# Kernel optimization log

Measured on AMD Instinct MI355X. Metric: run time of the kernel, lower is better.

Reference implementation:

```python
import jax, jax.numpy as jnp
import numpy as np

LOG_2PI = np.float32(np.log(2.0 * np.pi))
NEG_BIG = np.float32(-9e15)


def setup_inputs() -> dict:
    key = jax.random.key(0)
    ks = jax.random.split(key, 8)
    N, F_in, F_out, H = 8192, 512, 128, 16
    x = jax.random.normal(ks[0], (N, F_in), dtype=jnp.float32)
    adj = jax.random.randint(ks[1], (N, N), 0, 2, dtype=jnp.int32)
    # xavier_uniform-ish init for W (gain 1.414)
    lim = np.float32(1.414 * np.sqrt(6.0 / (F_in + F_out)))
    W = jax.random.uniform(ks[2], (F_in, F_out), jnp.float32, -lim, lim)
    # VariationalAttentionNet params: lin1(2*F_out -> H), lin21/lin22(H -> 1)
    w1 = jax.random.normal(ks[3], (H, 2 * F_out), dtype=jnp.float32) * 0.05
    b1 = jnp.zeros((H,), jnp.float32)
    w21 = jax.random.normal(ks[4], (1, H), dtype=jnp.float32) * 0.05
    b21 = jnp.zeros((1,), jnp.float32)
    w22 = jax.random.normal(ks[5], (1, H), dtype=jnp.float32) * 0.05
    b22 = jnp.zeros((1,), jnp.float32)
    return {"x": x, "adj": adj, "W": W, "w1": w1, "b1": b1,
            "w21": w21, "b21": b21, "w22": w22, "b22": b22}


def reference(x, adj, W, w1, b1, w21, b21, w22, b22):
    # h = x @ W  [N, F_out]
    h = x @ W
    # VariationalAttentionNet(h, h), eval mode: z = mu
    u = jax.nn.relu(jnp.concatenate([h, h], axis=1) @ w1.T + b1)  # [N, H]
    mu = u @ w21.T + b21   # [N, 1]
    lv = u @ w22.T + b22   # [N, 1]
    sigma = jax.nn.softplus(lv)
    z = mu
    # qmp = -(log p(z) - log q(z)); with z = mu, log q(mu) = -log(sigma) - 0.5*log(2pi)
    log_p = jnp.sum(-0.5 * z * z - 0.5 * LOG_2PI)
    log_q = jnp.sum(-jnp.log(sigma) - 0.5 * LOG_2PI)
    qmp = log_q - log_p
    # per-node score z broadcast across row, masked by adjacency, row softmax
    scores = jnp.where(adj > 0, z, NEG_BIG)          # [N, N]
    attention = jax.nn.softmax(scores, axis=1)       # [N, N] (dropout off in eval)
    h_prime = attention @ h                          # [N, F_out]
    return jax.nn.elu(h_prime), qmp
```

## Files before the change

### kernel.cpp

```cpp
#include <hip/hip_runtime.h>

typedef unsigned int u32;
typedef unsigned short u16;

#define NN 8192
#define FIN 512
#define FOUT 128
#define NH 16
#define BK 64
#define BKA 256

typedef float f32x16 __attribute__((ext_vector_type(16)));
typedef __bf16 bf16x8 __attribute__((ext_vector_type(8)));

union PackAB { u32 u[4]; bf16x8 v; };

__device__ __forceinline__ u32 rne_hi(u32 u) {
  return u + (0x7FFFu + ((u >> 16) & 1u));
}
__device__ __forceinline__ u16 f32_to_bf16(float f) {
  return (u16)(rne_hi(__float_as_uint(f)) >> 16);
}

__global__ __launch_bounds__(256) void prep_kernel(
    const float* __restrict__ W, const float* __restrict__ w1,
    u16* __restrict__ WT, float* __restrict__ w1s) {
  int b = blockIdx.x, t = threadIdx.x;
  if (b < 256) {
    int o = b * 256 + t;
    int n = o >> 9, k = o & 511;
    WT[o] = f32_to_bf16(W[k * FOUT + n]);
  } else {
    for (int e = t; e < NH * FOUT; e += 256) {
      int k = e >> 7, f = e & 127;
      w1s[e] = w1[k * 256 + f] + w1[k * 256 + 128 + f];
    }
  }
}

__global__ __launch_bounds__(256, 6) void h_kernel(
    const float* __restrict__ x, const u16* __restrict__ WT,
    float* __restrict__ Hp, int KL) {
  __shared__ u16 aS[32 * BK];
  __shared__ u16 bS[128 * BK];
  int t = threadIdx.x;
  int w = t >> 6, l = t & 63;
  int m = l & 31, kh = l >> 5;
  int tile = blockIdx.x & 255, chunk = blockIdx.x >> 8;
  int i0 = tile * 32, k0 = chunk * KL;

  int arow = t >> 4, acol = (t & 15) * 4;
  int ac = (t & 15) >> 1, ah = t & 1;
  int aoff0 = arow * BK + ((ac ^ (arow & 7)) << 3) + ah * 4;
  int aoff1 = (arow + 16) * BK + ((ac ^ ((arow + 16) & 7)) << 3) + ah * 4;
  const float* ap0 = x + (size_t)(i0 + arow) * FIN + k0 + acol;
  const float* ap1 = ap0 + (size_t)16 * FIN;
  int hr = t >> 3, hc = t & 7;
  const u16* bp0 = WT + (size_t)hr * FIN + k0 + hc * 8;
  int boff[4];
#pragma unroll
  for (int p = 0; p < 4; ++p) {
    int r = hr + 32 * p;
    boff[p] = r * BK + ((hc ^ (r & 7)) << 3);
  }
  int aro = m * BK, am7 = m & 7;
  int nB = w * 32 + m;
  int bro = nB * BK, bm7 = nB & 7;

  f32x16 acc;
#pragma unroll
  for (int r = 0; r < 16; ++r) acc[r] = 0.0f;

  for (int o = 0; o < KL; o += BK) {
    float4 a0 = *(const float4*)ap0;
    float4 a1 = *(const float4*)ap1;
    uint4 h0 = *(const uint4*)bp0;
    uint4 h1 = *(const uint4*)(bp0 + 32 * (size_t)FIN);
    uint4 h2 = *(const uint4*)(bp0 + 64 * (size_t)FIN);
    uint4 h3 = *(const uint4*)(bp0 + 96 * (size_t)FIN);
    ap0 += BK; ap1 += BK; bp0 += BK;
    uint2 w0, w1v;
    w0.x = (rne_hi(__float_as_uint(a0.y)) & 0xFFFF0000u) | (rne_hi(__float_as_uint(a0.x)) >> 16);
    w0.y = (rne_hi(__float_as_uint(a0.w)) & 0xFFFF0000u) | (rne_hi(__float_as_uint(a0.z)) >> 16);
    w1v.x = (rne_hi(__float_as_uint(a1.y)) & 0xFFFF0000u) | (rne_hi(__float_as_uint(a1.x)) >> 16);
    w1v.y = (rne_hi(__float_as_uint(a1.w)) & 0xFFFF0000u) | (rne_hi(__float_as_uint(a1.z)) >> 16);
    *(uint2*)&aS[aoff0] = w0;
    *(uint2*)&aS[aoff1] = w1v;
    *(uint4*)&bS[boff[0]] = h0;
    *(uint4*)&bS[boff[1]] = h1;
    *(uint4*)&bS[boff[2]] = h2;
    *(uint4*)&bS[boff[3]] = h3;
    __syncthreads();
#pragma unroll
    for (int s = 0; s < BK; s += 16) {
      int cA = (s >> 3) + kh;
      PackAB pa, pb;
      pa.v = *(const bf16x8*)&aS[aro + ((cA ^ am7) << 3)];
      pb.v = *(const bf16x8*)&bS[bro + ((cA ^ bm7) << 3)];
      acc = __builtin_amdgcn_mfma_f32_32x32x16_bf16(pa.v, pb.v, acc, 0, 0, 0);
    }
    __syncthreads();
  }
  float* hp = Hp + (size_t)chunk * NN * FOUT;
  int col = w * 32 + m;
#pragma unroll
  for (int r = 0; r < 16; ++r) {
    int row = (r & 3) + 8 * (r >> 2) + 4 * kh;
    hp[(size_t)(i0 + row) * FOUT + col] = acc[r];
  }
}

__global__ __launch_bounds__(256) void reduceH_kernel(
    const float* __restrict__ Hp, int KSH,
    const float* __restrict__ b1, const float* __restrict__ w21,
    const float* __restrict__ b21, const float* __restrict__ w22,
    const float* __restrict__ b22, const float* __restrict__ w1s,
    u16* __restrict__ HTf, float* __restrict__ qpart) {
  __shared__ float hs[32][FOUT + 4];
  __shared__ float w1l[NH][FOUT + 4];
  __shared__ float us[32][NH + 1];
  int t = threadIdx.x;
  int i0 = blockIdx.x * 32;
  float v[16];
  const float* base = Hp + (size_t)i0 * FOUT + t * 16;
#pragma unroll
  for (int e = 0; e < 16; e += 4) {
    float4 x4 = *(const float4*)(base + e);
    v[e] = x4.x; v[e + 1] = x4.y; v[e + 2] = x4.z; v[e + 3] = x4.w;
  }
  for (int c = 1; c < KSH; ++c) {
    const float* p = base + (size_t)c * NN * FOUT;
#pragma unroll
    for (int e = 0; e < 16; e += 4) {
      float4 x4 = *(const float4*)(p + e);
      v[e] += x4.x; v[e + 1] += x4.y; v[e + 2] += x4.z; v[e + 3] += x4.w;
    }
  }
  {
    int row = t >> 3, c0 = (t & 7) * 16;
#pragma unroll
    for (int e = 0; e < 16; ++e) hs[row][c0 + e] = v[e];
  }
  for (int e = t; e < NH * FOUT; e += 256) w1l[e >> 7][e & 127] = w1s[e];
  __syncthreads();
  {
    int n = t & 127, g2 = t >> 7;
#pragma unroll
    for (int gg = 0; gg < 2; ++gg) {
      int g = g2 + 2 * gg;
      int k16 = (i0 >> 4) + (g >> 1), kh = g & 1;
      u32 p[4];
#pragma unroll
      for (int j = 0; j < 4; ++j) {
        u16 lo = f32_to_bf16(hs[g * 8 + 2 * j][n]);
        u16 hi = f32_to_bf16(hs[g * 8 + 2 * j + 1][n]);
        p[j] = (u32)lo | ((u32)hi << 16);
      }
      uint4 st; st.x = p[0]; st.y = p[1]; st.z = p[2]; st.w = p[3];
      size_t off = ((size_t)(k16 * 4 + (n >> 5)) * 64 + kh * 32 + (n & 31)) * 8;
      *(uint4*)(HTf + off) = st;
    }
  }
  {
    int i = t >> 3, p = t & 7;
    float s0 = b1[p], s1 = b1[p + 8];
#pragma unroll 4
    for (int f = 0; f < FOUT; ++f) {
      float hv = hs[i][f];
      s0 = fmaf(hv, w1l[p][f], s0);
      s1 = fmaf(hv, w1l[p + 8][f], s1);
    }
    us[i][p] = fmaxf(s0, 0.0f);
    us[i][p + 8] = fmaxf(s1, 0.0f);
  }
  __syncthreads();
  if (t < 32) {
    float mu = b21[0], lv = b22[0];
#pragma unroll
    for (int k = 0; k < NH; ++k) {
      mu = fmaf(us[t][k], w21[k], mu);
      lv = fmaf(us[t][k], w22[k], lv);
    }
    float sp = fmaxf(lv, 0.0f) + log1pf(expf(-fabsf(lv)));
    float q = 0.5f * mu * mu - logf(sp);
#pragma unroll
    for (int off = 16; off; off >>= 1) q += __shfl_down(q, off);
    if (t == 0) qpart[blockIdx.x] = q;
  }
}

__global__ __launch_bounds__(256, 4) void attn_kernel(
    const int* __restrict__ adj, const u16* __restrict__ HTf,
    float* __restrict__ Sp, u32* __restrict__ degw, int KL) {
  __shared__ u16 aS[32 * BKA];
  int t = threadIdx.x;
  int w = t >> 6, l = t & 63;
  int m = l & 31, kh = l >> 5;
  int tile = blockIdx.x & 255, chunk = blockIdx.x >> 8;
  int i0 = tile * 32, k0 = chunk * KL;

  int ar = t >> 3, lc = t & 7;
  const int* apb = adj + (size_t)(i0 + ar) * NN + k0 + lc * 4;
  int woff[8];
#pragma unroll
  for (int q = 0; q < 8; ++q) {
    int c = q * 4 + (lc >> 1);
    woff[q] = ar * 256 + (((c ^ ar) & 31) << 3) + (lc & 1) * 4;
  }
  const u16* bp = HTf + ((size_t)(k0 >> 4) * 4 * 64 + (size_t)(w * 64 + l)) * 8;

  f32x16 acc;
#pragma unroll
  for (int r = 0; r < 16; ++r) acc[r] = 0.0f;
  u32 degacc = 0;

  int nslab = KL / BKA;
  int4 aC[8], aN[8];
#pragma unroll
  for (int q = 0; q < 8; ++q) aC[q] = *(const int4*)(apb + q * 32);
  apb += BKA;

  for (int o = 0; o < nslab; ++o) {
    if (o) __syncthreads();
#pragma unroll
    for (int q = 0; q < 8; ++q) {
      u32 p0 = ((u32)aC[q].y << 16) | (u32)aC[q].x;
      u32 p1 = ((u32)aC[q].w << 16) | (u32)aC[q].z;
      degacc += p0 + p1;
      uint2 wv; wv.x = p0 * 0x3F80u; wv.y = p1 * 0x3F80u;
      *(uint2*)&aS[woff[q]] = wv;
    }
    __syncthreads();
    if (o + 1 < nslab) {
#pragma unroll
      for (int q = 0; q < 8; ++q) aN[q] = *(const int4*)(apb + q * 32);
      apb += BKA;
    }
    {
      bf16x8 bF[4];
#pragma unroll
      for (int j = 0; j < 4; ++j) bF[j] = *(const bf16x8*)(bp + j * 2048);
#pragma unroll
      for (int k16 = 0; k16 < 16; k16 += 4) {
        bf16x8 bN[4];
        if (k16 + 4 < 16) {
#pragma unroll
          for (int j = 0; j < 4; ++j)
            bN[j] = *(const bf16x8*)(bp + (k16 + 4 + j) * 2048);
        }
#pragma unroll
        for (int j = 0; j < 4; ++j) {
          int cc = (k16 + j) * 2 + kh;
          PackAB pa;
          pa.v = *(const bf16x8*)&aS[m * 256 + (((cc ^ m) & 31) << 3)];
          acc = __builtin_amdgcn_mfma_f32_32x32x16_bf16(pa.v, bF[j], acc, 0, 0, 0);
        }
#pragma unroll
        for (int j = 0; j < 4; ++j) bF[j] = bN[j];
      }
    }
    bp += (size_t)16 * 2048;
#pragma unroll
    for (int q = 0; q < 8; ++q) aC[q] = aN[q];
  }
  u32 d = (degacc & 0xFFFFu) + (degacc >> 16);
  d += __shfl_down(d, 4);
  d += __shfl_down(d, 2);
  d += __shfl_down(d, 1);
  if (lc == 0) degw[chunk * NN + i0 + ar] = d;
  float* sp = Sp + (size_t)chunk * NN * FOUT;
  int col = w * 32 + m;
#pragma unroll
  for (int r = 0; r < 16; ++r) {
    int row = (r & 3) + 8 * (r >> 2) + 4 * kh;
    sp[(size_t)(i0 + row) * FOUT + col] = acc[r];
  }
}

__global__ __launch_bounds__(256) void reduceSq_kernel(
    const float* __restrict__ Sp, const u32* __restrict__ degw,
    const float* __restrict__ qpart, float* __restrict__ out, int KSA) {
  int t = threadIdx.x;
  if (blockIdx.x == 1024) {
    __shared__ float sred[4];
    float v = qpart[t];
#pragma unroll
    for (int off = 32; off; off >>= 1) v += __shfl_down(v, off);
    if ((t & 63) == 0) sred[t >> 6] = v;
    __syncthreads();
    if (t == 0) out[(size_t)NN * FOUT] = sred[0] + sred[1] + sred[2] + sred[3];
    return;
  }
  int idx = (blockIdx.x * 256 + t) * 4;
  int i = idx >> 7;
  u32 deg = 0;
  for (int c = 0; c < KSA; ++c) deg += degw[c * NN + i];
  float4 s = {0.0f, 0.0f, 0.0f, 0.0f};
  for (int c = 0; c < KSA; ++c) {
    float4 v4 = *(const float4*)(Sp + (size_t)c * NN * FOUT + idx);
    s.x += v4.x; s.y += v4.y; s.z += v4.z; s.w += v4.w;
  }
  float rd = deg ? 1.0f / (float)deg : 0.0f;
  float4 o;
  o.x = s.x * rd; o.y = s.y * rd; o.z = s.z * rd; o.w = s.w * rd;
  o.x = o.x > 0.0f ? o.x : expm1f(o.x);
  o.y = o.y > 0.0f ? o.y : expm1f(o.y);
  o.z = o.z > 0.0f ? o.z : expm1f(o.z);
  o.w = o.w > 0.0f ? o.w : expm1f(o.w);
  *(float4*)(out + idx) = o;
}

extern "C" void kernel_launch(void* const* d_in, const int* in_sizes, int n_in,
                              void* d_out, int out_size, void* d_ws, size_t ws_size,
                              hipStream_t stream) {
  (void)in_sizes; (void)n_in; (void)out_size;
  const float* x   = (const float*)d_in[0];
  const int*   adj = (const int*)d_in[1];
  const float* W   = (const float*)d_in[2];
  const float* w1  = (const float*)d_in[3];
  const float* b1  = (const float*)d_in[4];
  const float* w21 = (const float*)d_in[5];
  const float* b21 = (const float*)d_in[6];
  const float* w22 = (const float*)d_in[7];
  const float* b22 = (const float*)d_in[8];
  float* out = (float*)d_out;

  const size_t TILE4 = (size_t)NN * FOUT * 4;
  int KSA = 4, KSH = 4;
  for (;;) {
    size_t need = (size_t)(KSA + KSH) * TILE4
                + (size_t)NN * FOUT * 2
                + (size_t)FOUT * FIN * 2
                + (size_t)KSA * NN * 4
                + NH * FOUT * 4 + 2048;
    if (need <= ws_size || (KSA == 1 && KSH == 1)) break;
    if (KSH > 1) KSH >>= 1; else KSA >>= 1;
  }

  char* ws = (char*)d_ws;
  float* Sp   = (float*)ws;                          ws += (size_t)KSA * TILE4;
  float* Hp   = (float*)ws;                          ws += (size_t)KSH * TILE4;
  u16*   HTf  = (u16*)ws;                            ws += (size_t)NN * FOUT * 2;
  u16*   WT   = (u16*)ws;                            ws += (size_t)FOUT * FIN * 2;
  u32*   degw = (u32*)ws;                            ws += (size_t)KSA * NN * 4;
  float* w1s  = (float*)ws;                          ws += NH * FOUT * 4;
  float* qpart= (float*)ws;

  prep_kernel<<<257, 256, 0, stream>>>(W, w1, WT, w1s);
  h_kernel<<<256 * KSH, 256, 0, stream>>>(x, WT, Hp, FIN / KSH);
  reduceH_kernel<<<256, 256, 0, stream>>>(Hp, KSH, b1, w21, b21, w22, b22, w1s, HTf, qpart);
  attn_kernel<<<256 * KSA, 256, 0, stream>>>(adj, HTf, Sp, degw, NN / KSA);
  reduceSq_kernel<<<1025, 256, 0, stream>>>(Sp, degw, qpart, out, KSA);
}
```

Before: 419.0 us.

## Drop split-K partials and fuse reductions into the GEMM and attention kernels

```diff
diff --git a/kernel.cpp b/kernel.cpp
--- a/kernel.cpp
+++ b/kernel.cpp
@@ -38,25 +38,31 @@
   }
 }
 
-__global__ __launch_bounds__(256, 6) void h_kernel(
+__global__ __launch_bounds__(256) void h_fused_kernel(
     const float* __restrict__ x, const u16* __restrict__ WT,
-    float* __restrict__ Hp, int KL) {
-  __shared__ u16 aS[32 * BK];
-  __shared__ u16 bS[128 * BK];
+    const float* __restrict__ b1, const float* __restrict__ w21,
+    const float* __restrict__ b21, const float* __restrict__ w22,
+    const float* __restrict__ b22, const float* __restrict__ w1s,
+    u16* __restrict__ HTf, float* __restrict__ qpart) {
+  __shared__ union {
+    struct { u16 aS[32 * BK]; u16 bS[128 * BK]; } g;
+    float hs[32][FOUT + 4];
+  } S;
+  __shared__ float w1l[NH][FOUT + 4];
+  __shared__ float us[32][NH + 1];
   int t = threadIdx.x;
   int w = t >> 6, l = t & 63;
   int m = l & 31, kh = l >> 5;
-  int tile = blockIdx.x & 255, chunk = blockIdx.x >> 8;
-  int i0 = tile * 32, k0 = chunk * KL;
+  int i0 = blockIdx.x * 32;
 
   int arow = t >> 4, acol = (t & 15) * 4;
   int ac = (t & 15) >> 1, ah = t & 1;
   int aoff0 = arow * BK + ((ac ^ (arow & 7)) << 3) + ah * 4;
   int aoff1 = (arow + 16) * BK + ((ac ^ ((arow + 16) & 7)) << 3) + ah * 4;
-  const float* ap0 = x + (size_t)(i0 + arow) * FIN + k0 + acol;
+  const float* ap0 = x + (size_t)(i0 + arow) * FIN + acol;
   const float* ap1 = ap0 + (size_t)16 * FIN;
   int hr = t >> 3, hc = t & 7;
-  const u16* bp0 = WT + (size_t)hr * FIN + k0 + hc * 8;
+  const u16* bp0 = WT + (size_t)hr * FIN + hc * 8;
   int boff[4];
 #pragma unroll
   for (int p = 0; p < 4; ++p) {
@@ -67,79 +73,60 @@
   int nB = w * 32 + m;
   int bro = nB * BK, bm7 = nB & 7;
 
+  float4 xa[8], xb[8];
+#pragma unroll
+  for (int o = 0; o < 8; ++o) {
+    xa[o] = *(const float4*)(ap0 + o * BK);
+    xb[o] = *(const float4*)(ap1 + o * BK);
+  }
+  uint4 hC[4], hN[4];
+#pragma unroll
+  for (int j = 0; j < 4; ++j) hC[j] = *(const uint4*)(bp0 + (size_t)(32 * j) * FIN);
+  bp0 += BK;
+
   f32x16 acc;
 #pragma unroll
   for (int r = 0; r < 16; ++r) acc[r] = 0.0f;
 
-  for (int o = 0; o < KL; o += BK) {
-    float4 a0 = *(const float4*)ap0;
-    float4 a1 = *(const float4*)ap1;
-    uint4 h0 = *(const uint4*)bp0;
-    uint4 h1 = *(const uint4*)(bp0 + 32 * (size_t)FIN);
-    uint4 h2 = *(const uint4*)(bp0 + 64 * (size_t)FIN);
-    uint4 h3 = *(const uint4*)(bp0 + 96 * (size_t)FIN);
-    ap0 += BK; ap1 += BK; bp0 += BK;
+#pragma unroll
+  for (int o = 0; o < 8; ++o) {
+    if (o) __syncthreads();
     uint2 w0, w1v;
-    w0.x = (rne_hi(__float_as_uint(a0.y)) & 0xFFFF0000u) | (rne_hi(__float_as_uint(a0.x)) >> 16);
-    w0.y = (rne_hi(__float_as_uint(a0.w)) & 0xFFFF0000u) | (rne_hi(__float_as_uint(a0.z)) >> 16);
-    w1v.x = (rne_hi(__float_as_uint(a1.y)) & 0xFFFF0000u) | (rne_hi(__float_as_uint(a1.x)) >> 16);
-    w1v.y = (rne_hi(__float_as_uint(a1.w)) & 0xFFFF0000u) | (rne_hi(__float_as_uint(a1.z)) >> 16);
-    *(uint2*)&aS[aoff0] = w0;
-    *(uint2*)&aS[aoff1] = w1v;
-    *(uint4*)&bS[boff[0]] = h0;
-    *(uint4*)&bS[boff[1]] = h1;
-    *(uint4*)&bS[boff[2]] = h2;
-    *(uint4*)&bS[boff[3]] = h3;
+    w0.x = (rne_hi(__float_as_uint(xa[o].y)) & 0xFFFF0000u) | (rne_hi(__float_as_uint(xa[o].x)) >> 16);
+    w0.y = (rne_hi(__float_as_uint(xa[o].w)) & 0xFFFF0000u) | (rne_hi(__float_as_uint(xa[o].z)) >> 16);
+    w1v.x = (rne_hi(__float_as_uint(xb[o].y)) & 0xFFFF0000u) | (rne_hi(__float_as_uint(xb[o].x)) >> 16);
+    w1v.y = (rne_hi(__float_as_uint(xb[o].w)) & 0xFFFF0000u) | (rne_hi(__float_as_uint(xb[o].z)) >> 16);
+    *(uint2*)&S.g.aS[aoff0] = w0;
+    *(uint2*)&S.g.aS[aoff1] = w1v;
+#pragma unroll
+    for (int j = 0; j < 4; ++j) *(uint4*)&S.g.bS[boff[j]] = hC[j];
     __syncthreads();
+    if (o + 1 < 8) {
+#pragma unroll
+      for (int j = 0; j < 4; ++j) hN[j] = *(const uint4*)(bp0 + (size_t)(32 * j) * FIN);
+      bp0 += BK;
+    }
 #pragma unroll
     for (int s = 0; s < BK; s += 16) {
       int cA = (s >> 3) + kh;
       PackAB pa, pb;
-      pa.v = *(const bf16x8*)&aS[aro + ((cA ^ am7) << 3)];
-      pb.v = *(const bf16x8*)&bS[bro + ((cA ^ bm7) << 3)];
+      pa.v = *(const bf16x8*)&S.g.aS[aro + ((cA ^ am7) << 3)];
+      pb.v = *(const bf16x8*)&S.g.bS[bro + ((cA ^ bm7) << 3)];
       acc = __builtin_amdgcn_mfma_f32_32x32x16_bf16(pa.v, pb.v, acc, 0, 0, 0);
     }
-    __syncthreads();
-  }
-  float* hp = Hp + (size_t)chunk * NN * FOUT;
-  int col = w * 32 + m;
-#pragma unroll
-  for (int r = 0; r < 16; ++r) {
-    int row = (r & 3) + 8 * (r >> 2) + 4 * kh;
-    hp[(size_t)(i0 + row) * FOUT + col] = acc[r];
-  }
-}
-
-__global__ __launch_bounds__(256) void reduceH_kernel(
-    const float* __restrict__ Hp, int KSH,
-    const float* __restrict__ b1, const float* __restrict__ w21,
-    const float* __restrict__ b21, const float* __restrict__ w22,
-    const float* __restrict__ b22, const float* __restrict__ w1s,
-    u16* __restrict__ HTf, float* __restrict__ qpart) {
-  __shared__ float hs[32][FOUT + 4];
-  __shared__ float w1l[NH][FOUT + 4];
-  __shared__ float us[32][NH + 1];
-  int t = threadIdx.x;
-  int i0 = blockIdx.x * 32;
-  float v[16];
-  const float* base = Hp + (size_t)i0 * FOUT + t * 16;
-#pragma unroll
-  for (int e = 0; e < 16; e += 4) {
-    float4 x4 = *(const float4*)(base + e);
-    v[e] = x4.x; v[e + 1] = x4.y; v[e + 2] = x4.z; v[e + 3] = x4.w;
-  }
-  for (int c = 1; c < KSH; ++c) {
-    const float* p = base + (size_t)c * NN * FOUT;
-#pragma unroll
-    for (int e = 0; e < 16; e += 4) {
-      float4 x4 = *(const float4*)(p + e);
-      v[e] += x4.x; v[e + 1] += x4.y; v[e + 2] += x4.z; v[e + 3] += x4.w;
-    }
-  }
+    if (o + 1 < 8) {
+#pragma unroll
+      for (int j = 0; j < 4; ++j) hC[j] = hN[j];
+    }
+  }
+  __syncthreads();
   {
-    int row = t >> 3, c0 = (t & 7) * 16;
-#pragma unroll
-    for (int e = 0; e < 16; ++e) hs[row][c0 + e] = v[e];
+    int col = w * 32 + m;
+#pragma unroll
+    for (int r = 0; r < 16; ++r) {
+      int row = (r & 3) + 8 * (r >> 2) + 4 * kh;
+      S.hs[row][col] = acc[r];
+    }
   }
   for (int e = t; e < NH * FOUT; e += 256) w1l[e >> 7][e & 127] = w1s[e];
   __syncthreads();
@@ -148,16 +135,16 @@
 #pragma unroll
     for (int gg = 0; gg < 2; ++gg) {
       int g = g2 + 2 * gg;
-      int k16 = (i0 >> 4) + (g >> 1), kh = g & 1;
+      int k16 = (i0 >> 4) + (g >> 1), khh = g & 1;
       u32 p[4];
 #pragma unroll
       for (int j = 0; j < 4; ++j) {
-        u16 lo = f32_to_bf16(hs[g * 8 + 2 * j][n]);
-        u16 hi = f32_to_bf16(hs[g * 8 + 2 * j + 1][n]);
+        u16 lo = f32_to_bf16(S.hs[g * 8 + 2 * j][n]);
+        u16 hi = f32_to_bf16(S.hs[g * 8 + 2 * j + 1][n]);
         p[j] = (u32)lo | ((u32)hi << 16);
       }
       uint4 st; st.x = p[0]; st.y = p[1]; st.z = p[2]; st.w = p[3];
-      size_t off = ((size_t)(k16 * 4 + (n >> 5)) * 64 + kh * 32 + (n & 31)) * 8;
+      size_t off = ((size_t)(k16 * 4 + (n >> 5)) * 64 + khh * 32 + (n & 31)) * 8;
       *(uint4*)(HTf + off) = st;
     }
   }
@@ -166,7 +153,7 @@
     float s0 = b1[p], s1 = b1[p + 8];
 #pragma unroll 4
     for (int f = 0; f < FOUT; ++f) {
-      float hv = hs[i][f];
+      float hv = S.hs[i][f];
       s0 = fmaf(hv, w1l[p][f], s0);
       s1 = fmaf(hv, w1l[p + 8][f], s1);
     }
@@ -189,32 +176,32 @@
   }
 }
 
-__global__ __launch_bounds__(256, 4) void attn_kernel(
+__global__ __launch_bounds__(256) void attn_kernel(
     const int* __restrict__ adj, const u16* __restrict__ HTf,
-    float* __restrict__ Sp, u32* __restrict__ degw, int KL) {
+    const float* __restrict__ qpart, float* __restrict__ out) {
   __shared__ u16 aS[32 * BKA];
+  __shared__ float dinv[32];
   int t = threadIdx.x;
   int w = t >> 6, l = t & 63;
   int m = l & 31, kh = l >> 5;
-  int tile = blockIdx.x & 255, chunk = blockIdx.x >> 8;
-  int i0 = tile * 32, k0 = chunk * KL;
+  int i0 = blockIdx.x * 32;
 
   int ar = t >> 3, lc = t & 7;
-  const int* apb = adj + (size_t)(i0 + ar) * NN + k0 + lc * 4;
+  const int* apb = adj + (size_t)(i0 + ar) * NN + lc * 4;
   int woff[8];
 #pragma unroll
   for (int q = 0; q < 8; ++q) {
     int c = q * 4 + (lc >> 1);
     woff[q] = ar * 256 + (((c ^ ar) & 31) << 3) + (lc & 1) * 4;
   }
-  const u16* bp = HTf + ((size_t)(k0 >> 4) * 4 * 64 + (size_t)(w * 64 + l)) * 8;
+  const u16* bp = HTf + (size_t)(w * 64 + l) * 8;
 
   f32x16 acc;
 #pragma unroll
   for (int r = 0; r < 16; ++r) acc[r] = 0.0f;
   u32 degacc = 0;
 
-  int nslab = KL / BKA;
+  const int nslab = NN / BKA;
   int4 aC[8], aN[8];
 #pragma unroll
   for (int q = 0; q < 8; ++q) aC[q] = *(const int4*)(apb + q * 32);
@@ -267,53 +254,28 @@
   d += __shfl_down(d, 4);
   d += __shfl_down(d, 2);
   d += __shfl_down(d, 1);
-  if (lc == 0) degw[chunk * NN + i0 + ar] = d;
-  float* sp = Sp + (size_t)chunk * NN * FOUT;
+  if (lc == 0) dinv[ar] = d ? 1.0f / (float)d : 0.0f;
+  __syncthreads();
   int col = w * 32 + m;
 #pragma unroll
   for (int r = 0; r < 16; ++r) {
     int row = (r & 3) + 8 * (r >> 2) + 4 * kh;
-    sp[(size_t)(i0 + row) * FOUT + col] = acc[r];
-  }
-}
-
-__global__ __launch_bounds__(256) void reduceSq_kernel(
-    const float* __restrict__ Sp, const u32* __restrict__ degw,
-    const float* __restrict__ qpart, float* __restrict__ out, int KSA) {
-  int t = threadIdx.x;
-  if (blockIdx.x == 1024) {
-    __shared__ float sred[4];
-    float v = qpart[t];
+    float v = acc[r] * dinv[row];
+    v = v > 0.0f ? v : expm1f(v);
+    out[(size_t)(i0 + row) * FOUT + col] = v;
+  }
+  if (blockIdx.x == 0 && t < 64) {
+    float v = qpart[t] + qpart[t + 64] + qpart[t + 128] + qpart[t + 192];
 #pragma unroll
     for (int off = 32; off; off >>= 1) v += __shfl_down(v, off);
-    if ((t & 63) == 0) sred[t >> 6] = v;
-    __syncthreads();
-    if (t == 0) out[(size_t)NN * FOUT] = sred[0] + sred[1] + sred[2] + sred[3];
-    return;
-  }
-  int idx = (blockIdx.x * 256 + t) * 4;
-  int i = idx >> 7;
-  u32 deg = 0;
-  for (int c = 0; c < KSA; ++c) deg += degw[c * NN + i];
-  float4 s = {0.0f, 0.0f, 0.0f, 0.0f};
-  for (int c = 0; c < KSA; ++c) {
-    float4 v4 = *(const float4*)(Sp + (size_t)c * NN * FOUT + idx);
-    s.x += v4.x; s.y += v4.y; s.z += v4.z; s.w += v4.w;
-  }
-  float rd = deg ? 1.0f / (float)deg : 0.0f;
-  float4 o;
-  o.x = s.x * rd; o.y = s.y * rd; o.z = s.z * rd; o.w = s.w * rd;
-  o.x = o.x > 0.0f ? o.x : expm1f(o.x);
-  o.y = o.y > 0.0f ? o.y : expm1f(o.y);
-  o.z = o.z > 0.0f ? o.z : expm1f(o.z);
-  o.w = o.w > 0.0f ? o.w : expm1f(o.w);
-  *(float4*)(out + idx) = o;
+    if (t == 0) out[(size_t)NN * FOUT] = v;
+  }
 }
 
 extern "C" void kernel_launch(void* const* d_in, const int* in_sizes, int n_in,
                               void* d_out, int out_size, void* d_ws, size_t ws_size,
                               hipStream_t stream) {
-  (void)in_sizes; (void)n_in; (void)out_size;
+  (void)in_sizes; (void)n_in; (void)out_size; (void)ws_size;
   const float* x   = (const float*)d_in[0];
   const int*   adj = (const int*)d_in[1];
   const float* W   = (const float*)d_in[2];
@@ -325,30 +287,13 @@
   const float* b22 = (const float*)d_in[8];
   float* out = (float*)d_out;
 
-  const size_t TILE4 = (size_t)NN * FOUT * 4;
-  int KSA = 4, KSH = 4;
-  for (;;) {
-    size_t need = (size_t)(KSA + KSH) * TILE4
-                + (size_t)NN * FOUT * 2
-                + (size_t)FOUT * FIN * 2
-                + (size_t)KSA * NN * 4
-                + NH * FOUT * 4 + 2048;
-    if (need <= ws_size || (KSA == 1 && KSH == 1)) break;
-    if (KSH > 1) KSH >>= 1; else KSA >>= 1;
-  }
-
   char* ws = (char*)d_ws;
-  float* Sp   = (float*)ws;                          ws += (size_t)KSA * TILE4;
-  float* Hp   = (float*)ws;                          ws += (size_t)KSH * TILE4;
-  u16*   HTf  = (u16*)ws;                            ws += (size_t)NN * FOUT * 2;
-  u16*   WT   = (u16*)ws;                            ws += (size_t)FOUT * FIN * 2;
-  u32*   degw = (u32*)ws;                            ws += (size_t)KSA * NN * 4;
-  float* w1s  = (float*)ws;                          ws += NH * FOUT * 4;
+  u16*   HTf  = (u16*)ws;   ws += (size_t)NN * FOUT * 2;
+  u16*   WT   = (u16*)ws;   ws += (size_t)FOUT * FIN * 2;
+  float* w1s  = (float*)ws; ws += NH * FOUT * 4;
   float* qpart= (float*)ws;
 
   prep_kernel<<<257, 256, 0, stream>>>(W, w1, WT, w1s);
-  h_kernel<<<256 * KSH, 256, 0, stream>>>(x, WT, Hp, FIN / KSH);
-  reduceH_kernel<<<256, 256, 0, stream>>>(Hp, KSH, b1, w21, b21, w22, b22, w1s, HTf, qpart);
-  attn_kernel<<<256 * KSA, 256, 0, stream>>>(adj, HTf, Sp, degw, NN / KSA);
-  reduceSq_kernel<<<1025, 256, 0, stream>>>(Sp, degw, qpart, out, KSA);
-}
+  h_fused_kernel<<<256, 256, 0, stream>>>(x, WT, b1, w21, b21, w22, b22, w1s, HTf, qpart);
+  attn_kernel<<<256, 256, 0, stream>>>(adj, HTf, qpart, out);
+}
```

Result: slower. 505.9 us (+20.7%).
